# Optimization experiments

Measured on AMD Instinct MI355X. Metric: run time of the kernel, lower is better.

Reference implementation:

```python
import jax, jax.numpy as jnp
import numpy as np

N, E, G = 10000, 160000, 64
F, C1, C2, C3, K, NC = 128, 128, 256, 512, 5, 10


def setup_inputs() -> dict:
    key = jax.random.key(0)
    ks = jax.random.split(key, 12)
    s = 0.05
    return {
        "x": jax.random.normal(ks[0], (N, F), dtype=jnp.float32),
        "edge_index": jax.random.randint(ks[1], (2, E), 0, N, dtype=jnp.int64),
        "batch": jnp.sort(jax.random.randint(ks[2], (N,), 0, G, dtype=jnp.int64)),
        "W_cheb": jax.random.normal(ks[3], (K, F, C1), dtype=jnp.float32) * s,
        "b_cheb": jnp.zeros((C1,), jnp.float32),
        "W_g1": jax.random.normal(ks[4], (C1, C2), dtype=jnp.float32) * s,
        "b_g1": jnp.zeros((C2,), jnp.float32),
        "W_g2": jax.random.normal(ks[5], (C2, C3), dtype=jnp.float32) * s,
        "b_g2": jnp.zeros((C3,), jnp.float32),
        "w_gate": jax.random.normal(ks[6], (C3, 1), dtype=jnp.float32) * s,
        "b_gate": jnp.zeros((1,), jnp.float32),
        "W_fc": jax.random.normal(ks[7], (C3, NC), dtype=jnp.float32) * s,
        "b_fc": jnp.zeros((NC,), jnp.float32),
    }


def _deg_inv_sqrt(deg):
    return jnp.where(deg > 0, jax.lax.rsqrt(jnp.maximum(deg, 1e-12)), 0.0)


def cheb_conv(x, src, dst, W, b):
    # PyG ChebConv, sym normalization, lambda_max=2 => scaled Laplacian = -D^-1/2 A D^-1/2
    ones = jnp.ones((src.shape[0],), x.dtype)
    deg = jax.ops.segment_sum(ones, src, num_segments=N)
    dinv = _deg_inv_sqrt(deg)
    w = -(dinv[src] * dinv[dst])  # [E]

    def prop(h):
        return jax.ops.segment_sum(w[:, None] * h[src], dst, num_segments=N)

    tx0 = x
    tx1 = prop(x)
    out = tx0 @ W[0] + tx1 @ W[1]
    for k in range(2, W.shape[0]):
        tx2 = 2.0 * prop(tx1) - tx0
        out = out + tx2 @ W[k]
        tx0, tx1 = tx1, tx2
    return out + b


def gcn_conv(x, src, dst, W, b):
    # PyG GCNConv: add self-loops, sym norm D~^-1/2 (A+I) D~^-1/2, transform then aggregate
    loop = jnp.arange(N, dtype=src.dtype)
    src_a = jnp.concatenate([src, loop])
    dst_a = jnp.concatenate([dst, loop])
    ones = jnp.ones((src_a.shape[0],), x.dtype)
    deg = jax.ops.segment_sum(ones, dst_a, num_segments=N)
    dinv = _deg_inv_sqrt(deg)
    norm = dinv[src_a] * dinv[dst_a]  # [E+N]
    h = x @ W
    return jax.ops.segment_sum(norm[:, None] * h[src_a], dst_a, num_segments=N) + b


def attention_pool(x, batch, w_gate, b_gate):
    logits = (x @ w_gate + b_gate)[:, 0]  # [N]
    m = jax.ops.segment_max(logits, batch, num_segments=G)
    e = jnp.exp(logits - m[batch])
    s = jax.ops.segment_sum(e, batch, num_segments=G)
    alpha = e / s[batch]
    return jax.ops.segment_sum(alpha[:, None] * x, batch, num_segments=G)  # [G, C3]


def reference(x, edge_index, batch, W_cheb, b_cheb, W_g1, b_g1, W_g2, b_g2,
              w_gate, b_gate, W_fc, b_fc):
    src, dst = edge_index[0], edge_index[1]
    h = jax.nn.relu(cheb_conv(x, src, dst, W_cheb, b_cheb))
    h = jax.nn.relu(gcn_conv(h, src, dst, W_g1, b_g1))
    h = jax.nn.relu(gcn_conv(h, src, dst, W_g2, b_g2))
    g = attention_pool(h, batch, w_gate, b_gate)
    logits = g @ W_fc + b_fc
    return jax.nn.log_softmax(logits, axis=1)
```

## Files before the change

### kernel.cpp

```cpp
#include <hip/hip_runtime.h>
#include <hip/hip_bf16.h>
#include <math.h>

#define N_NODES 10000
#define N_EDGES 160000
#define N_GRAPHS 64
#define F_IN    128
#define C1_DIM  128
#define C2_DIM  256
#define C3_DIM  512
#define K_CHEB  5
#define NCLS    10
#define TC      (K_CHEB * F_IN)

typedef short v8s __attribute__((ext_vector_type(8)));
typedef float v4f __attribute__((ext_vector_type(4)));

static __device__ __forceinline__ unsigned short f2bf(float f) {
    unsigned u = __float_as_uint(f);
    unsigned r = (u + 0x7FFFu + ((u >> 16) & 1u)) >> 16;
    return (unsigned short)r;
}
static __device__ __forceinline__ float bf_lo(unsigned u) { return __uint_as_float(u << 16); }
static __device__ __forceinline__ float bf_hi(unsigned u) { return __uint_as_float(u & 0xFFFF0000u); }

__global__ void count_kernel(const int* __restrict__ src, const int* __restrict__ dst,
                             int* __restrict__ cnt_s, int* __restrict__ cnt_d, int E) {
    int e = blockIdx.x * blockDim.x + threadIdx.x;
    if (e >= E) return;
    atomicAdd(&cnt_s[src[e]], 1);
    atomicAdd(&cnt_d[dst[e]], 1);
}

__global__ __launch_bounds__(256) void scan_dinv_kernel(
        const int* __restrict__ cnt_s, const int* __restrict__ cnt_d,
        int* __restrict__ rowptr, float* __restrict__ dinv_c, float* __restrict__ dinv_g, int n) {
    __shared__ int sums[256];
    int tid = threadIdx.x;
    int chunk = (n + 255) / 256;
    int s0 = tid * chunk, s1 = min(n, s0 + chunk);
    int loc = 0;
    for (int i = s0; i < s1; i++) {
        int cd = cnt_d[i];
        loc += cd;
        int cs = cnt_s[i];
        dinv_c[i] = (cs > 0) ? rsqrtf((float)cs) : 0.0f;
        dinv_g[i] = rsqrtf((float)cd + 1.0f);
    }
    sums[tid] = loc;
    __syncthreads();
    for (int off = 1; off < 256; off <<= 1) {
        int t = (tid >= off) ? sums[tid - off] : 0;
        __syncthreads();
        sums[tid] += t;
        __syncthreads();
    }
    int pre = sums[tid] - loc;
    for (int i = s0; i < s1; i++) { rowptr[i] = pre; pre += cnt_d[i]; }
    if (tid == 255) rowptr[n] = pre;
}

__global__ void fill_kernel(const int* __restrict__ src, const int* __restrict__ dst,
                            const float* __restrict__ dinv_c, const float* __restrict__ dinv_g,
                            const int* __restrict__ rowptr, int* __restrict__ fillc,
                            int* __restrict__ col, float* __restrict__ wch,
                            float* __restrict__ nrm, int E) {
    int e = blockIdx.x * blockDim.x + threadIdx.x;
    if (e >= E) return;
    int s = src[e], d = dst[e];
    int pos = rowptr[d] + atomicAdd(&fillc[d], 1);
    col[pos] = s;
    wch[pos] = -(dinv_c[s] * dinv_c[d]);
    nrm[pos] = dinv_g[s] * dinv_g[d];
}

#define PREP_A (N_NODES * 64)
#define PREP_B (TC * C1_DIM)
#define PREP_C (C1_DIM * C2_DIM)
#define PREP_D (C2_DIM * C3_DIM)
#define PREP_TOTAL (PREP_A + PREP_B + PREP_C + PREP_D + N_NODES)
__global__ void prep_kernel(const float* __restrict__ x, unsigned short* __restrict__ tcat,
                            const float* __restrict__ Wcheb, unsigned short* __restrict__ Wcb_t,
                            const float* __restrict__ Wg1, unsigned short* __restrict__ Wg1_t,
                            const float* __restrict__ Wg2, unsigned short* __restrict__ Wg2_t,
                            const int* __restrict__ batch, int* __restrict__ gptr) {
    int id = blockIdx.x * blockDim.x + threadIdx.x;
    if (id < PREP_A) {
        int n = id >> 6, f = (id & 63) * 2;
        float2 v = *(const float2*)(x + (size_t)n * F_IN + f);
        ushort2 o; o.x = f2bf(v.x); o.y = f2bf(v.y);
        *(ushort2*)(tcat + (size_t)n * TC + f) = o;
        return;
    }
    id -= PREP_A;
    if (id < PREP_B) {
        int n = id % C1_DIM, k = id / C1_DIM;
        Wcb_t[(size_t)n * TC + k] = f2bf(Wcheb[(size_t)k * C1_DIM + n]);
        return;
    }
    id -= PREP_B;
    if (id < PREP_C) {
        int n = id % C2_DIM, k = id / C2_DIM;
        Wg1_t[(size_t)n * C1_DIM + k] = f2bf(Wg1[(size_t)k * C2_DIM + n]);
        return;
    }
    id -= PREP_C;
    if (id < PREP_D) {
        int n = id % C3_DIM, k = id / C3_DIM;
        Wg2_t[(size_t)n * C2_DIM + k] = f2bf(Wg2[(size_t)k * C3_DIM + n]);
        return;
    }
    id -= PREP_D;
    int i = id;
    int b = batch[i];
    if (i == 0) { for (int g = 0; g <= b; g++) gptr[g] = 0; }
    else {
        int bp = batch[i - 1];
        for (int g = bp + 1; g <= b; g++) gptr[g] = i;
    }
    if (i == N_NODES - 1) { for (int g = b + 1; g <= N_GRAPHS; g++) gptr[g] = N_NODES; }
}

__global__ __launch_bounds__(256) void gather_cheb_bf(
        const unsigned short* __restrict__ tb,
        const int* __restrict__ rowptr, const int* __restrict__ col,
        const float* __restrict__ ew,
        const unsigned short* __restrict__ base,
        float alpha, float beta,
        unsigned short* __restrict__ outc,
        int n) {
    int w = (blockIdx.x * blockDim.x + threadIdx.x) >> 6;
    int lane = threadIdx.x & 63;
    if (w >= n) return;
    float a0 = 0.0f, a1 = 0.0f;
    int rs = rowptr[w], re = rowptr[w + 1];
    for (int b = rs; b < re; b += 64) {
        int cl = 0; float wl = 0.0f;
        if (b + lane < re) { cl = col[b + lane]; wl = ew[b + lane]; }
        int nk4 = (min(64, re - b) + 3) & ~3;
        for (int j = 0; j < nk4; j += 4) {
            int s0 = __shfl(cl, j), s1 = __shfl(cl, j + 1);
            int s2 = __shfl(cl, j + 2), s3 = __shfl(cl, j + 3);
            float w0 = __shfl(wl, j), w1 = __shfl(wl, j + 1);
            float w2 = __shfl(wl, j + 2), w3 = __shfl(wl, j + 3);
            unsigned u0 = ((const unsigned*)(tb + (size_t)s0 * TC))[lane];
            unsigned u1 = ((const unsigned*)(tb + (size_t)s1 * TC))[lane];
            unsigned u2 = ((const unsigned*)(tb + (size_t)s2 * TC))[lane];
            unsigned u3 = ((const unsigned*)(tb + (size_t)s3 * TC))[lane];
            a0 += w0 * bf_lo(u0) + w1 * bf_lo(u1) + w2 * bf_lo(u2) + w3 * bf_lo(u3);
            a1 += w0 * bf_hi(u0) + w1 * bf_hi(u1) + w2 * bf_hi(u2) + w3 * bf_hi(u3);
        }
    }
    if (base) {
        unsigned ub = ((const unsigned*)(base + (size_t)w * TC))[lane];
        a0 = alpha * a0 + beta * bf_lo(ub);
        a1 = alpha * a1 + beta * bf_hi(ub);
    } else {
        a0 *= alpha; a1 *= alpha;
    }
    ushort2 o; o.x = f2bf(a0); o.y = f2bf(a1);
    *(ushort2*)(outc + (size_t)w * TC + lane * 2) = o;
}

template<int FPL>
__global__ __launch_bounds__(256) void gather_gcn_pre(
        const unsigned short* __restrict__ tb, const int* __restrict__ rowptr,
        const int* __restrict__ col, const float* __restrict__ ew,
        const float* __restrict__ dinv, unsigned short* __restrict__ z, int n) {
    const int C = FPL * 64;
    int w = (blockIdx.x * blockDim.x + threadIdx.x) >> 6;
    int lane = threadIdx.x & 63;
    if (w >= n) return;
    float acc[FPL];
    #pragma unroll
    for (int q = 0; q < FPL; q++) acc[q] = 0.0f;
    int rs = rowptr[w], re = rowptr[w + 1];
    for (int b = rs; b < re; b += 64) {
        int cl = 0; float wl = 0.0f;
        if (b + lane < re) { cl = col[b + lane]; wl = ew[b + lane]; }
        int nk4 = (min(64, re - b) + 3) & ~3;
        for (int j = 0; j < nk4; j += 4) {
            int s0 = __shfl(cl, j), s1 = __shfl(cl, j + 1);
            int s2 = __shfl(cl, j + 2), s3 = __shfl(cl, j + 3);
            float w0 = __shfl(wl, j), w1 = __shfl(wl, j + 1);
            float w2 = __shfl(wl, j + 2), w3 = __shfl(wl, j + 3);
            if constexpr (FPL == 2) {
                unsigned u0 = ((const unsigned*)(tb + (size_t)s0 * C))[lane];
                unsigned u1 = ((const unsigned*)(tb + (size_t)s1 * C))[lane];
                unsigned u2 = ((const unsigned*)(tb + (size_t)s2 * C))[lane];
                unsigned u3 = ((const unsigned*)(tb + (size_t)s3 * C))[lane];
                acc[0] += w0 * bf_lo(u0) + w1 * bf_lo(u1) + w2 * bf_lo(u2) + w3 * bf_lo(u3);
                acc[1] += w0 * bf_hi(u0) + w1 * bf_hi(u1) + w2 * bf_hi(u2) + w3 * bf_hi(u3);
            } else {
                uint2 u0 = ((const uint2*)(tb + (size_t)s0 * C))[lane];
                uint2 u1 = ((const uint2*)(tb + (size_t)s1 * C))[lane];
                uint2 u2 = ((const uint2*)(tb + (size_t)s2 * C))[lane];
                uint2 u3 = ((const uint2*)(tb + (size_t)s3 * C))[lane];
                acc[0] += w0 * bf_lo(u0.x) + w1 * bf_lo(u1.x) + w2 * bf_lo(u2.x) + w3 * bf_lo(u3.x);
                acc[1] += w0 * bf_hi(u0.x) + w1 * bf_hi(u1.x) + w2 * bf_hi(u2.x) + w3 * bf_hi(u3.x);
                acc[2] += w0 * bf_lo(u0.y) + w1 * bf_lo(u1.y) + w2 * bf_lo(u2.y) + w3 * bf_lo(u3.y);
                acc[3] += w0 * bf_hi(u0.y) + w1 * bf_hi(u1.y) + w2 * bf_hi(u2.y) + w3 * bf_hi(u3.y);
            }
        }
    }
    float sn = dinv[w] * dinv[w];
    if constexpr (FPL == 2) {
        unsigned u = ((const unsigned*)(tb + (size_t)w * C))[lane];
        acc[0] += sn * bf_lo(u); acc[1] += sn * bf_hi(u);
        ushort2 o; o.x = f2bf(acc[0]); o.y = f2bf(acc[1]);
        *(ushort2*)(z + (size_t)w * C + lane * 2) = o;
    } else {
        uint2 u = ((const uint2*)(tb + (size_t)w * C))[lane];
        acc[0] += sn * bf_lo(u.x); acc[1] += sn * bf_hi(u.x);
        acc[2] += sn * bf_lo(u.y); acc[3] += sn * bf_hi(u.y);
        ushort4 o; o.x = f2bf(acc[0]); o.y = f2bf(acc[1]);
        o.z = f2bf(acc[2]); o.w = f2bf(acc[3]);
        *(ushort4*)(z + (size_t)w * C + lane * 4) = o;
    }
}

__global__ __launch_bounds__(256) void gemm_bf16(
        const unsigned short* __restrict__ A, const unsigned short* __restrict__ Bt,
        const float* __restrict__ bias, float* __restrict__ Cf,
        unsigned short* __restrict__ Cb, int M, int K, int N, int relu) {
    int m0 = blockIdx.y * 64, n0 = blockIdx.x * 128;
    int wave = threadIdx.x >> 6, lane = threadIdx.x & 63;
    int wm = (wave & 1) * 32, wn = (wave >> 1) * 64;
    int l15 = lane & 15, quad = lane >> 4;

    v4f acc[2][4];
    #pragma unroll
    for (int i = 0; i < 2; i++)
        #pragma unroll
        for (int j = 0; j < 4; j++) acc[i][j] = (v4f){0.f, 0.f, 0.f, 0.f};

    const unsigned short* Ab[2]; bool av[2];
    #pragma unroll
    for (int i = 0; i < 2; i++) {
        int row = m0 + wm + i * 16 + l15;
        av[i] = row < M;
        Ab[i] = A + (size_t)(av[i] ? row : 0) * K + quad * 8;
    }
    const unsigned short* Bb[4];
    #pragma unroll
    for (int j = 0; j < 4; j++) {
        int coln = n0 + wn + j * 16 + l15;
        Bb[j] = Bt + (size_t)coln * K + quad * 8;
    }
    const v8s zero8 = {0, 0, 0, 0, 0, 0, 0, 0};

    for (int k0 = 0; k0 < K; k0 += 32) {
        v8s a[2], b[4];
        #pragma unroll
        for (int i = 0; i < 2; i++) a[i] = av[i] ? *(const v8s*)(Ab[i] + k0) : zero8;
        #pragma unroll
        for (int j = 0; j < 4; j++) b[j] = *(const v8s*)(Bb[j] + k0);
        #pragma unroll
        for (int i = 0; i < 2; i++)
            #pragma unroll
            for (int j = 0; j < 4; j++)
                acc[i][j] = __builtin_amdgcn_mfma_f32_16x16x32_bf16(a[i], b[j], acc[i][j], 0, 0, 0);
    }

    #pragma unroll
    for (int j = 0; j < 4; j++) {
        int coln = n0 + wn + j * 16 + l15;
        float bv = bias ? bias[coln] : 0.0f;
        #pragma unroll
        for (int i = 0; i < 2; i++) {
            int rbase = m0 + wm + i * 16 + quad * 4;
            #pragma unroll
            for (int r = 0; r < 4; r++) {
                int row = rbase + r;
                if (row >= M) continue;
                float v = acc[i][j][r] + bv;
                if (relu) v = fmaxf(v, 0.0f);
                if (Cf) Cf[(size_t)row * N + coln] = v;
                else    Cb[(size_t)row * N + coln] = f2bf(v);
            }
        }
    }
}

__global__ void gate_kernel(const float* __restrict__ h3, const float* __restrict__ wg,
                            const float* __restrict__ bg, float* __restrict__ logits, int n) {
    int node = blockIdx.x * 4 + (threadIdx.x >> 6);
    int lane = threadIdx.x & 63;
    if (node >= n) return;
    float s = 0.0f;
    #pragma unroll
    for (int i = 0; i < 8; i++) {
        int c = i * 64 + lane;
        s += h3[(size_t)node * C3_DIM + c] * wg[c];
    }
    #pragma unroll
    for (int off = 32; off > 0; off >>= 1) s += __shfl_down(s, off);
    if (lane == 0) logits[node] = s + bg[0];
}

__global__ __launch_bounds__(256) void pool_stats(float* __restrict__ logits,
                                                  const int* __restrict__ gptr,
                                                  float* __restrict__ pooled) {
    __shared__ float red[256];
    int g = blockIdx.x, tid = threadIdx.x;
    int gs = gptr[g], ge = gptr[g + 1];
    pooled[(size_t)g * C3_DIM + tid] = 0.0f;
    pooled[(size_t)g * C3_DIM + 256 + tid] = 0.0f;
    float m = -INFINITY;
    for (int i = gs + tid; i < ge; i += 256) m = fmaxf(m, logits[i]);
    red[tid] = m; __syncthreads();
    for (int off = 128; off > 0; off >>= 1) {
        if (tid < off) red[tid] = fmaxf(red[tid], red[tid + off]);
        __syncthreads();
    }
    m = red[0]; __syncthreads();
    float s = 0.0f;
    for (int i = gs + tid; i < ge; i += 256) s += expf(logits[i] - m);
    red[tid] = s; __syncthreads();
    for (int off = 128; off > 0; off >>= 1) {
        if (tid < off) red[tid] += red[tid + off];
        __syncthreads();
    }
    s = red[0];
    float sinv = (s > 0.0f) ? 1.0f / s : 0.0f;
    for (int i = gs + tid; i < ge; i += 256)
        logits[i] = expf(logits[i] - m) * sinv;
}

__global__ __launch_bounds__(256) void pool_partial(const float* __restrict__ h3,
        const float* __restrict__ alpha, const int* __restrict__ gptr,
        float* __restrict__ pooled) {
    int g = blockIdx.x, ch = blockIdx.y, sl = blockIdx.z;
    int gs = gptr[g], ge = gptr[g + 1];
    int cnt = ge - gs;
    int i0 = gs + (cnt * sl) / 8;
    int i1 = gs + (cnt * (sl + 1)) / 8;
    int c = ch * 256 + threadIdx.x;
    float acc = 0.0f;
    for (int i = i0; i < i1; i++)
        acc += alpha[i] * h3[(size_t)i * C3_DIM + c];
    if (i1 > i0) atomicAdd(&pooled[(size_t)g * C3_DIM + c], acc);
}

__global__ void fc_kernel(const float* __restrict__ pooled, const float* __restrict__ Wfc,
                          const float* __restrict__ bfc, float* __restrict__ out) {
    int g = blockIdx.x;
    int t = threadIdx.x;
    float acc = -INFINITY;
    if (t < NCLS) {
        acc = bfc[t];
        for (int k = 0; k < C3_DIM; k++)
            acc += pooled[(size_t)g * C3_DIM + k] * Wfc[k * NCLS + t];
    }
    float m = acc;
    #pragma unroll
    for (int off = 8; off > 0; off >>= 1) m = fmaxf(m, __shfl_xor(m, off, 16));
    float e = (t < NCLS) ? expf(acc - m) : 0.0f;
    float s = e;
    #pragma unroll
    for (int off = 8; off > 0; off >>= 1) s += __shfl_xor(s, off, 16);
    if (t < NCLS) out[g * NCLS + t] = acc - m - logf(s);
}

extern "C" void kernel_launch(void* const* d_in, const int* in_sizes, int n_in,
                              void* d_out, int out_size, void* d_ws, size_t ws_size,
                              hipStream_t stream) {
    const float* x      = (const float*)d_in[0];
    const int*   ei     = (const int*)d_in[1];
    const int*   batch  = (const int*)d_in[2];
    const float* W_cheb = (const float*)d_in[3];
    const float* b_cheb = (const float*)d_in[4];
    const float* W_g1   = (const float*)d_in[5];
    const float* b_g1   = (const float*)d_in[6];
    const float* W_g2   = (const float*)d_in[7];
    const float* b_g2   = (const float*)d_in[8];
    const float* w_gate = (const float*)d_in[9];
    const float* b_gate = (const float*)d_in[10];
    const float* W_fc   = (const float*)d_in[11];
    const float* b_fc   = (const float*)d_in[12];
    const int* src = ei;
    const int* dst = ei + N_EDGES;
    float* out = (float*)d_out;

    const int N = N_NODES, E = N_EDGES, G = N_GRAPHS;

    char* Wp = (char*)d_ws;
    auto alloc = [&](size_t bytes) {
        void* p = Wp;
        Wp += (bytes + 255) & ~(size_t)255;
        return p;
    };
    int*   cnt3    = (int*)alloc((size_t)3 * N * 4);
    int*   cnt_s   = cnt3;
    int*   cnt_d   = cnt3 + N;
    int*   fillc   = cnt3 + 2 * N;
    int*   rowptr  = (int*)alloc((N + 1) * 4);
    int*   col     = (int*)alloc(E * 4);
    float* wch     = (float*)alloc(E * 4);
    float* nrm     = (float*)alloc(E * 4);
    float* dinv_c  = (float*)alloc(N * 4);
    float* dinv_g  = (float*)alloc(N * 4);
    unsigned short* tcat  = (unsigned short*)alloc((size_t)N * TC * 2);
    unsigned short* h1b   = (unsigned short*)alloc((size_t)N * C1_DIM * 2);
    unsigned short* z1b   = (unsigned short*)alloc((size_t)N * C1_DIM * 2);
    unsigned short* h2b   = (unsigned short*)alloc((size_t)N * C2_DIM * 2);
    unsigned short* z2b   = (unsigned short*)alloc((size_t)N * C2_DIM * 2);
    float* h3      = (float*)alloc((size_t)N * C3_DIM * 4);
    unsigned short* Wcb_t = (unsigned short*)alloc((size_t)TC * C1_DIM * 2);
    unsigned short* Wg1_t = (unsigned short*)alloc((size_t)C1_DIM * C2_DIM * 2);
    unsigned short* Wg2_t = (unsigned short*)alloc((size_t)C2_DIM * C3_DIM * 2);
    float* logits  = (float*)alloc(N * 4);
    int*   gptr    = (int*)alloc((G + 1) * 4);
    float* pooled  = (float*)alloc((size_t)G * C3_DIM * 4);

    dim3 blk(256);
    auto cdiv = [](int a, int b) { return (a + b - 1) / b; };

    hipLaunchKernelGGL(prep_kernel, dim3(cdiv(PREP_TOTAL, 256)), blk, 0, stream,
                       x, tcat, W_cheb, Wcb_t, W_g1, Wg1_t, W_g2, Wg2_t, batch, gptr);

    hipMemsetAsync(cnt3, 0, (size_t)3 * N * sizeof(int), stream);
    hipLaunchKernelGGL(count_kernel, dim3(cdiv(E, 256)), blk, 0, stream, src, dst, cnt_s, cnt_d, E);
    hipLaunchKernelGGL(scan_dinv_kernel, dim3(1), blk, 0, stream, cnt_s, cnt_d, rowptr, dinv_c, dinv_g, N);
    hipLaunchKernelGGL(fill_kernel, dim3(cdiv(E, 256)), blk, 0, stream,
                       src, dst, dinv_c, dinv_g, rowptr, fillc, col, wch, nrm, E);

    const int NWB = cdiv(N, 4);

    hipLaunchKernelGGL(gather_cheb_bf, dim3(NWB), blk, 0, stream,
                       tcat + 0 * F_IN, rowptr, col, wch,
                       (const unsigned short*)nullptr, 1.0f, 0.0f, tcat + 1 * F_IN, N);
    hipLaunchKernelGGL(gather_cheb_bf, dim3(NWB), blk, 0, stream,
                       tcat + 1 * F_IN, rowptr, col, wch,
                       tcat + 0 * F_IN, 2.0f, -1.0f, tcat + 2 * F_IN, N);
    hipLaunchKernelGGL(gather_cheb_bf, dim3(NWB), blk, 0, stream,
                       tcat + 2 * F_IN, rowptr, col, wch,
                       tcat + 1 * F_IN, 2.0f, -1.0f, tcat + 3 * F_IN, N);
    hipLaunchKernelGGL(gather_cheb_bf, dim3(NWB), blk, 0, stream,
                       tcat + 3 * F_IN, rowptr, col, wch,
                       tcat + 2 * F_IN, 2.0f, -1.0f, tcat + 4 * F_IN, N);

    hipLaunchKernelGGL(gemm_bf16, dim3(C1_DIM / 128, cdiv(N, 64)), blk, 0, stream,
                       tcat, Wcb_t, b_cheb, (float*)nullptr, h1b, N, TC, C1_DIM, 1);

    hipLaunchKernelGGL(gather_gcn_pre<2>, dim3(NWB), blk, 0, stream,
                       h1b, rowptr, col, nrm, dinv_g, z1b, N);
    hipLaunchKernelGGL(gemm_bf16, dim3(C2_DIM / 128, cdiv(N, 64)), blk, 0, stream,
                       z1b, Wg1_t, b_g1, (float*)nullptr, h2b, N, C1_DIM, C2_DIM, 1);

    hipLaunchKernelGGL(gather_gcn_pre<4>, dim3(NWB), blk, 0, stream,
                       h2b, rowptr, col, nrm, dinv_g, z2b, N);
    hipLaunchKernelGGL(gemm_bf16, dim3(C3_DIM / 128, cdiv(N, 64)), blk, 0, stream,
                       z2b, Wg2_t, b_g2, h3, (unsigned short*)nullptr, N, C2_DIM, C3_DIM, 1);

    hipLaunchKernelGGL(gate_kernel, dim3(cdiv(N, 4)), blk, 0, stream, h3, w_gate, b_gate, logits, N);
    hipLaunchKernelGGL(pool_stats, dim3(G), blk, 0, stream, logits, gptr, pooled);
    hipLaunchKernelGGL(pool_partial, dim3(G, C3_DIM / 256, 8), blk, 0, stream,
                       h3, logits, gptr, pooled);

    hipLaunchKernelGGL(fc_kernel, dim3(G), dim3(64), 0, stream, pooled, W_fc, b_fc, out);
}
```

Before: 312.6 us.

## Fuse gate into GEMM epilogue, store h3 in bf16, merge degree counting into prep

Several changes at once. The edge degree counting and logits zeroing move into the prep kernel, and the scan now runs from LDS. The dinv arrays are dropped and degrees are computed on the fly in fill and gather. The gather loops are unrolled to 8 loads in flight. The GEMM is templated on column tiles, using a narrower tile for the first layer, and the final GEMM writes h3 as bf16 while computing the gate logits in its epilogue with atomics, which removes the separate gate kernel and halves h3 traffic in pooling. Risks: the gate bias is dropped (harmless here since softmax cancels it), atomic logit accumulation order varies, and bf16 h3 lowers pooling precision.

```diff
diff --git a/kernel.cpp b/kernel.cpp
--- a/kernel.cpp
+++ b/kernel.cpp
@@ -24,29 +24,81 @@
 static __device__ __forceinline__ float bf_lo(unsigned u) { return __uint_as_float(u << 16); }
 static __device__ __forceinline__ float bf_hi(unsigned u) { return __uint_as_float(u & 0xFFFF0000u); }
 
-__global__ void count_kernel(const int* __restrict__ src, const int* __restrict__ dst,
-                             int* __restrict__ cnt_s, int* __restrict__ cnt_d, int E) {
-    int e = blockIdx.x * blockDim.x + threadIdx.x;
-    if (e >= E) return;
-    atomicAdd(&cnt_s[src[e]], 1);
-    atomicAdd(&cnt_d[dst[e]], 1);
-}
-
-__global__ __launch_bounds__(256) void scan_dinv_kernel(
-        const int* __restrict__ cnt_s, const int* __restrict__ cnt_d,
-        int* __restrict__ rowptr, float* __restrict__ dinv_c, float* __restrict__ dinv_g, int n) {
+#define PREP_A (N_NODES * 64)
+#define PREP_B (TC * C1_DIM)
+#define PREP_C (C1_DIM * C2_DIM)
+#define PREP_D (C2_DIM * C3_DIM)
+#define PREP_E N_NODES
+#define PREP_F N_NODES
+#define PREP_G N_EDGES
+#define PREP_TOTAL (PREP_A + PREP_B + PREP_C + PREP_D + PREP_E + PREP_F + PREP_G)
+__global__ void prep_kernel(const float* __restrict__ x, unsigned short* __restrict__ tcat,
+                            const float* __restrict__ Wcheb, unsigned short* __restrict__ Wcb_t,
+                            const float* __restrict__ Wg1, unsigned short* __restrict__ Wg1_t,
+                            const float* __restrict__ Wg2, unsigned short* __restrict__ Wg2_t,
+                            const int* __restrict__ batch, int* __restrict__ gptr,
+                            float* __restrict__ logits,
+                            const int* __restrict__ src, const int* __restrict__ dst,
+                            int* __restrict__ cnt_s, int* __restrict__ cnt_d) {
+    int id = blockIdx.x * blockDim.x + threadIdx.x;
+    if (id < PREP_A) {
+        int n = id >> 6, f = (id & 63) * 2;
+        float2 v = *(const float2*)(x + (size_t)n * F_IN + f);
+        ushort2 o; o.x = f2bf(v.x); o.y = f2bf(v.y);
+        *(ushort2*)(tcat + (size_t)n * TC + f) = o;
+        return;
+    }
+    id -= PREP_A;
+    if (id < PREP_B) {
+        int n = id % C1_DIM, k = id / C1_DIM;
+        Wcb_t[(size_t)n * TC + k] = f2bf(Wcheb[(size_t)k * C1_DIM + n]);
+        return;
+    }
+    id -= PREP_B;
+    if (id < PREP_C) {
+        int n = id % C2_DIM, k = id / C2_DIM;
+        Wg1_t[(size_t)n * C1_DIM + k] = f2bf(Wg1[(size_t)k * C2_DIM + n]);
+        return;
+    }
+    id -= PREP_C;
+    if (id < PREP_D) {
+        int n = id % C3_DIM, k = id / C3_DIM;
+        Wg2_t[(size_t)n * C2_DIM + k] = f2bf(Wg2[(size_t)k * C3_DIM + n]);
+        return;
+    }
+    id -= PREP_D;
+    if (id < PREP_E) {
+        int i = id;
+        int b = batch[i];
+        if (i == 0) { for (int g = 0; g <= b; g++) gptr[g] = 0; }
+        else {
+            int bp = batch[i - 1];
+            for (int g = bp + 1; g <= b; g++) gptr[g] = i;
+        }
+        if (i == N_NODES - 1) { for (int g = b + 1; g <= N_GRAPHS; g++) gptr[g] = N_NODES; }
+        return;
+    }
+    id -= PREP_E;
+    if (id < PREP_F) { logits[id] = 0.0f; return; }
+    id -= PREP_F;
+    if (id < PREP_G) {
+        atomicAdd(&cnt_s[src[id]], 1);
+        atomicAdd(&cnt_d[dst[id]], 1);
+    }
+}
+
+__global__ __launch_bounds__(256) void scan_kernel(const int* __restrict__ cnt_d,
+                                                   int* __restrict__ rowptr, int n) {
+    __shared__ int ldsc[N_NODES];
     __shared__ int sums[256];
     int tid = threadIdx.x;
+    for (int i = tid; i < n; i += 256) ldsc[i] = cnt_d[i];
+    __syncthreads();
     int chunk = (n + 255) / 256;
     int s0 = tid * chunk, s1 = min(n, s0 + chunk);
+    if (s0 > n) s0 = n;
     int loc = 0;
-    for (int i = s0; i < s1; i++) {
-        int cd = cnt_d[i];
-        loc += cd;
-        int cs = cnt_s[i];
-        dinv_c[i] = (cs > 0) ? rsqrtf((float)cs) : 0.0f;
-        dinv_g[i] = rsqrtf((float)cd + 1.0f);
-    }
+    for (int i = s0; i < s1; i++) loc += ldsc[i];
     sums[tid] = loc;
     __syncthreads();
     for (int off = 1; off < 256; off <<= 1) {
@@ -56,12 +108,14 @@
         __syncthreads();
     }
     int pre = sums[tid] - loc;
-    for (int i = s0; i < s1; i++) { rowptr[i] = pre; pre += cnt_d[i]; }
+    for (int i = s0; i < s1; i++) { int v = ldsc[i]; ldsc[i] = pre; pre += v; }
+    __syncthreads();
+    for (int i = tid; i < n; i += 256) rowptr[i] = ldsc[i];
     if (tid == 255) rowptr[n] = pre;
 }
 
 __global__ void fill_kernel(const int* __restrict__ src, const int* __restrict__ dst,
-                            const float* __restrict__ dinv_c, const float* __restrict__ dinv_g,
+                            const int* __restrict__ cnt_s, const int* __restrict__ cnt_d,
                             const int* __restrict__ rowptr, int* __restrict__ fillc,
                             int* __restrict__ col, float* __restrict__ wch,
                             float* __restrict__ nrm, int E) {
@@ -70,65 +124,18 @@
     int s = src[e], d = dst[e];
     int pos = rowptr[d] + atomicAdd(&fillc[d], 1);
     col[pos] = s;
-    wch[pos] = -(dinv_c[s] * dinv_c[d]);
-    nrm[pos] = dinv_g[s] * dinv_g[d];
-}
-
-#define PREP_A (N_NODES * 64)
-#define PREP_B (TC * C1_DIM)
-#define PREP_C (C1_DIM * C2_DIM)
-#define PREP_D (C2_DIM * C3_DIM)
-#define PREP_TOTAL (PREP_A + PREP_B + PREP_C + PREP_D + N_NODES)
-__global__ void prep_kernel(const float* __restrict__ x, unsigned short* __restrict__ tcat,
-                            const float* __restrict__ Wcheb, unsigned short* __restrict__ Wcb_t,
-                            const float* __restrict__ Wg1, unsigned short* __restrict__ Wg1_t,
-                            const float* __restrict__ Wg2, unsigned short* __restrict__ Wg2_t,
-                            const int* __restrict__ batch, int* __restrict__ gptr) {
-    int id = blockIdx.x * blockDim.x + threadIdx.x;
-    if (id < PREP_A) {
-        int n = id >> 6, f = (id & 63) * 2;
-        float2 v = *(const float2*)(x + (size_t)n * F_IN + f);
-        ushort2 o; o.x = f2bf(v.x); o.y = f2bf(v.y);
-        *(ushort2*)(tcat + (size_t)n * TC + f) = o;
-        return;
-    }
-    id -= PREP_A;
-    if (id < PREP_B) {
-        int n = id % C1_DIM, k = id / C1_DIM;
-        Wcb_t[(size_t)n * TC + k] = f2bf(Wcheb[(size_t)k * C1_DIM + n]);
-        return;
-    }
-    id -= PREP_B;
-    if (id < PREP_C) {
-        int n = id % C2_DIM, k = id / C2_DIM;
-        Wg1_t[(size_t)n * C1_DIM + k] = f2bf(Wg1[(size_t)k * C2_DIM + n]);
-        return;
-    }
-    id -= PREP_C;
-    if (id < PREP_D) {
-        int n = id % C3_DIM, k = id / C3_DIM;
-        Wg2_t[(size_t)n * C2_DIM + k] = f2bf(Wg2[(size_t)k * C3_DIM + n]);
-        return;
-    }
-    id -= PREP_D;
-    int i = id;
-    int b = batch[i];
-    if (i == 0) { for (int g = 0; g <= b; g++) gptr[g] = 0; }
-    else {
-        int bp = batch[i - 1];
-        for (int g = bp + 1; g <= b; g++) gptr[g] = i;
-    }
-    if (i == N_NODES - 1) { for (int g = b + 1; g <= N_GRAPHS; g++) gptr[g] = N_NODES; }
+    int cs = cnt_s[s], cd = cnt_s[d];
+    float ds = (cs > 0) ? rsqrtf((float)cs) : 0.0f;
+    float dd = (cd > 0) ? rsqrtf((float)cd) : 0.0f;
+    wch[pos] = -(ds * dd);
+    nrm[pos] = rsqrtf((float)cnt_d[s] + 1.0f) * rsqrtf((float)cnt_d[d] + 1.0f);
 }
 
 __global__ __launch_bounds__(256) void gather_cheb_bf(
-        const unsigned short* __restrict__ tb,
-        const int* __restrict__ rowptr, const int* __restrict__ col,
-        const float* __restrict__ ew,
-        const unsigned short* __restrict__ base,
-        float alpha, float beta,
-        unsigned short* __restrict__ outc,
-        int n) {
+        const unsigned short* __restrict__ tb, const int* __restrict__ rowptr,
+        const int* __restrict__ col, const float* __restrict__ ew,
+        const unsigned short* __restrict__ base, float alpha, float beta,
+        unsigned short* __restrict__ outc, int n) {
     int w = (blockIdx.x * blockDim.x + threadIdx.x) >> 6;
     int lane = threadIdx.x & 63;
     if (w >= n) return;
@@ -137,18 +144,15 @@
     for (int b = rs; b < re; b += 64) {
         int cl = 0; float wl = 0.0f;
         if (b + lane < re) { cl = col[b + lane]; wl = ew[b + lane]; }
-        int nk4 = (min(64, re - b) + 3) & ~3;
-        for (int j = 0; j < nk4; j += 4) {
-            int s0 = __shfl(cl, j), s1 = __shfl(cl, j + 1);
-            int s2 = __shfl(cl, j + 2), s3 = __shfl(cl, j + 3);
-            float w0 = __shfl(wl, j), w1 = __shfl(wl, j + 1);
-            float w2 = __shfl(wl, j + 2), w3 = __shfl(wl, j + 3);
-            unsigned u0 = ((const unsigned*)(tb + (size_t)s0 * TC))[lane];
-            unsigned u1 = ((const unsigned*)(tb + (size_t)s1 * TC))[lane];
-            unsigned u2 = ((const unsigned*)(tb + (size_t)s2 * TC))[lane];
-            unsigned u3 = ((const unsigned*)(tb + (size_t)s3 * TC))[lane];
-            a0 += w0 * bf_lo(u0) + w1 * bf_lo(u1) + w2 * bf_lo(u2) + w3 * bf_lo(u3);
-            a1 += w0 * bf_hi(u0) + w1 * bf_hi(u1) + w2 * bf_hi(u2) + w3 * bf_hi(u3);
+        int nk8 = (min(64, re - b) + 7) & ~7;
+        for (int j = 0; j < nk8; j += 8) {
+            int ss[8]; float ww[8]; unsigned uu[8];
+            #pragma unroll
+            for (int q = 0; q < 8; q++) { ss[q] = __shfl(cl, j + q); ww[q] = __shfl(wl, j + q); }
+            #pragma unroll
+            for (int q = 0; q < 8; q++) uu[q] = ((const unsigned*)(tb + (size_t)ss[q] * TC))[lane];
+            #pragma unroll
+            for (int q = 0; q < 8; q++) { a0 += ww[q] * bf_lo(uu[q]); a1 += ww[q] * bf_hi(uu[q]); }
         }
     }
     if (base) {
@@ -166,7 +170,7 @@
 __global__ __launch_bounds__(256) void gather_gcn_pre(
         const unsigned short* __restrict__ tb, const int* __restrict__ rowptr,
         const int* __restrict__ col, const float* __restrict__ ew,
-        const float* __restrict__ dinv, unsigned short* __restrict__ z, int n) {
+        const int* __restrict__ cnt_d, unsigned short* __restrict__ z, int n) {
     const int C = FPL * 64;
     int w = (blockIdx.x * blockDim.x + threadIdx.x) >> 6;
     int lane = threadIdx.x & 63;
@@ -178,32 +182,33 @@
     for (int b = rs; b < re; b += 64) {
         int cl = 0; float wl = 0.0f;
         if (b + lane < re) { cl = col[b + lane]; wl = ew[b + lane]; }
-        int nk4 = (min(64, re - b) + 3) & ~3;
-        for (int j = 0; j < nk4; j += 4) {
-            int s0 = __shfl(cl, j), s1 = __shfl(cl, j + 1);
-            int s2 = __shfl(cl, j + 2), s3 = __shfl(cl, j + 3);
-            float w0 = __shfl(wl, j), w1 = __shfl(wl, j + 1);
-            float w2 = __shfl(wl, j + 2), w3 = __shfl(wl, j + 3);
+        int nk8 = (min(64, re - b) + 7) & ~7;
+        for (int j = 0; j < nk8; j += 8) {
+            int ss[8]; float ww[8];
+            #pragma unroll
+            for (int q = 0; q < 8; q++) { ss[q] = __shfl(cl, j + q); ww[q] = __shfl(wl, j + q); }
             if constexpr (FPL == 2) {
-                unsigned u0 = ((const unsigned*)(tb + (size_t)s0 * C))[lane];
-                unsigned u1 = ((const unsigned*)(tb + (size_t)s1 * C))[lane];
-                unsigned u2 = ((const unsigned*)(tb + (size_t)s2 * C))[lane];
-                unsigned u3 = ((const unsigned*)(tb + (size_t)s3 * C))[lane];
-                acc[0] += w0 * bf_lo(u0) + w1 * bf_lo(u1) + w2 * bf_lo(u2) + w3 * bf_lo(u3);
-                acc[1] += w0 * bf_hi(u0) + w1 * bf_hi(u1) + w2 * bf_hi(u2) + w3 * bf_hi(u3);
+                unsigned uu[8];
+                #pragma unroll
+                for (int q = 0; q < 8; q++) uu[q] = ((const unsigned*)(tb + (size_t)ss[q] * C))[lane];
+                #pragma unroll
+                for (int q = 0; q < 8; q++) {
+                    acc[0] += ww[q] * bf_lo(uu[q]);
+                    acc[1] += ww[q] * bf_hi(uu[q]);
+                }
             } else {
-                uint2 u0 = ((const uint2*)(tb + (size_t)s0 * C))[lane];
-                uint2 u1 = ((const uint2*)(tb + (size_t)s1 * C))[lane];
-                uint2 u2 = ((const uint2*)(tb + (size_t)s2 * C))[lane];
-                uint2 u3 = ((const uint2*)(tb + (size_t)s3 * C))[lane];
-                acc[0] += w0 * bf_lo(u0.x) + w1 * bf_lo(u1.x) + w2 * bf_lo(u2.x) + w3 * bf_lo(u3.x);
-                acc[1] += w0 * bf_hi(u0.x) + w1 * bf_hi(u1.x) + w2 * bf_hi(u2.x) + w3 * bf_hi(u3.x);
-                acc[2] += w0 * bf_lo(u0.y) + w1 * bf_lo(u1.y) + w2 * bf_lo(u2.y) + w3 * bf_lo(u3.y);
-                acc[3] += w0 * bf_hi(u0.y) + w1 * bf_hi(u1.y) + w2 * bf_hi(u2.y) + w3 * bf_hi(u3.y);
+                uint2 uu[8];
+                #pragma unroll
+                for (int q = 0; q < 8; q++) uu[q] = ((const uint2*)(tb + (size_t)ss[q] * C))[lane];
+                #pragma unroll
+                for (int q = 0; q < 8; q++) {
+                    acc[0] += ww[q] * bf_lo(uu[q].x); acc[1] += ww[q] * bf_hi(uu[q].x);
+                    acc[2] += ww[q] * bf_lo(uu[q].y); acc[3] += ww[q] * bf_hi(uu[q].y);
+                }
             }
         }
     }
-    float sn = dinv[w] * dinv[w];
+    float sn = 1.0f / (float)(cnt_d[w] + 1);
     if constexpr (FPL == 2) {
         unsigned u = ((const unsigned*)(tb + (size_t)w * C))[lane];
         acc[0] += sn * bf_lo(u); acc[1] += sn * bf_hi(u);
@@ -219,20 +224,22 @@
     }
 }
 
+template<int JT>
 __global__ __launch_bounds__(256) void gemm_bf16(
         const unsigned short* __restrict__ A, const unsigned short* __restrict__ Bt,
         const float* __restrict__ bias, float* __restrict__ Cf,
-        unsigned short* __restrict__ Cb, int M, int K, int N, int relu) {
-    int m0 = blockIdx.y * 64, n0 = blockIdx.x * 128;
+        unsigned short* __restrict__ Cb, const float* __restrict__ wg,
+        float* __restrict__ logits, int M, int K, int N, int relu) {
+    int m0 = blockIdx.y * 64, n0 = blockIdx.x * (JT * 32);
     int wave = threadIdx.x >> 6, lane = threadIdx.x & 63;
-    int wm = (wave & 1) * 32, wn = (wave >> 1) * 64;
+    int wm = (wave & 1) * 32, wn = (wave >> 1) * (JT * 16);
     int l15 = lane & 15, quad = lane >> 4;
 
-    v4f acc[2][4];
+    v4f acc[2][JT];
     #pragma unroll
     for (int i = 0; i < 2; i++)
         #pragma unroll
-        for (int j = 0; j < 4; j++) acc[i][j] = (v4f){0.f, 0.f, 0.f, 0.f};
+        for (int j = 0; j < JT; j++) acc[i][j] = (v4f){0.f, 0.f, 0.f, 0.f};
 
     const unsigned short* Ab[2]; bool av[2];
     #pragma unroll
@@ -241,61 +248,57 @@
         av[i] = row < M;
         Ab[i] = A + (size_t)(av[i] ? row : 0) * K + quad * 8;
     }
-    const unsigned short* Bb[4];
-    #pragma unroll
-    for (int j = 0; j < 4; j++) {
+    const unsigned short* Bb[JT];
+    #pragma unroll
+    for (int j = 0; j < JT; j++) {
         int coln = n0 + wn + j * 16 + l15;
         Bb[j] = Bt + (size_t)coln * K + quad * 8;
     }
     const v8s zero8 = {0, 0, 0, 0, 0, 0, 0, 0};
 
     for (int k0 = 0; k0 < K; k0 += 32) {
-        v8s a[2], b[4];
+        v8s a[2], b[JT];
         #pragma unroll
         for (int i = 0; i < 2; i++) a[i] = av[i] ? *(const v8s*)(Ab[i] + k0) : zero8;
         #pragma unroll
-        for (int j = 0; j < 4; j++) b[j] = *(const v8s*)(Bb[j] + k0);
+        for (int j = 0; j < JT; j++) b[j] = *(const v8s*)(Bb[j] + k0);
         #pragma unroll
         for (int i = 0; i < 2; i++)
             #pragma unroll
-            for (int j = 0; j < 4; j++)
+            for (int j = 0; j < JT; j++)
                 acc[i][j] = __builtin_amdgcn_mfma_f32_16x16x32_bf16(a[i], b[j], acc[i][j], 0, 0, 0);
     }
 
-    #pragma unroll
-    for (int j = 0; j < 4; j++) {
+    float bv[JT], wgj[JT];
+    #pragma unroll
+    for (int j = 0; j < JT; j++) {
         int coln = n0 + wn + j * 16 + l15;
-        float bv = bias ? bias[coln] : 0.0f;
+        bv[j] = bias[coln];
+        wgj[j] = wg ? wg[coln] : 0.0f;
+    }
+    #pragma unroll
+    for (int i = 0; i < 2; i++) {
         #pragma unroll
-        for (int i = 0; i < 2; i++) {
-            int rbase = m0 + wm + i * 16 + quad * 4;
-            #pragma unroll
-            for (int r = 0; r < 4; r++) {
-                int row = rbase + r;
-                if (row >= M) continue;
-                float v = acc[i][j][r] + bv;
+        for (int r = 0; r < 4; r++) {
+            int row = m0 + wm + i * 16 + quad * 4 + r;
+            if (row >= M) continue;
+            float gval = 0.0f;
+            #pragma unroll
+            for (int j = 0; j < JT; j++) {
+                int coln = n0 + wn + j * 16 + l15;
+                float v = acc[i][j][r] + bv[j];
                 if (relu) v = fmaxf(v, 0.0f);
                 if (Cf) Cf[(size_t)row * N + coln] = v;
                 else    Cb[(size_t)row * N + coln] = f2bf(v);
+                gval += v * wgj[j];
+            }
+            if (wg) {
+                #pragma unroll
+                for (int off = 1; off < 16; off <<= 1) gval += __shfl_xor(gval, off);
+                if (l15 == 0) atomicAdd(&logits[row], gval);
             }
         }
     }
-}
-
-__global__ void gate_kernel(const float* __restrict__ h3, const float* __restrict__ wg,
-                            const float* __restrict__ bg, float* __restrict__ logits, int n) {
-    int node = blockIdx.x * 4 + (threadIdx.x >> 6);
-    int lane = threadIdx.x & 63;
-    if (node >= n) return;
-    float s = 0.0f;
-    #pragma unroll
-    for (int i = 0; i < 8; i++) {
-        int c = i * 64 + lane;
-        s += h3[(size_t)node * C3_DIM + c] * wg[c];
-    }
-    #pragma unroll
-    for (int off = 32; off > 0; off >>= 1) s += __shfl_down(s, off);
-    if (lane == 0) logits[node] = s + bg[0];
 }
 
 __global__ __launch_bounds__(256) void pool_stats(float* __restrict__ logits,
@@ -327,19 +330,25 @@
         logits[i] = expf(logits[i] - m) * sinv;
 }
 
-__global__ __launch_bounds__(256) void pool_partial(const float* __restrict__ h3,
+__global__ __launch_bounds__(256) void pool_partial(const unsigned short* __restrict__ h3b,
         const float* __restrict__ alpha, const int* __restrict__ gptr,
         float* __restrict__ pooled) {
-    int g = blockIdx.x, ch = blockIdx.y, sl = blockIdx.z;
+    int g = blockIdx.x, sl = blockIdx.y, tid = threadIdx.x;
     int gs = gptr[g], ge = gptr[g + 1];
     int cnt = ge - gs;
     int i0 = gs + (cnt * sl) / 8;
     int i1 = gs + (cnt * (sl + 1)) / 8;
-    int c = ch * 256 + threadIdx.x;
-    float acc = 0.0f;
-    for (int i = i0; i < i1; i++)
-        acc += alpha[i] * h3[(size_t)i * C3_DIM + c];
-    if (i1 > i0) atomicAdd(&pooled[(size_t)g * C3_DIM + c], acc);
+    float a0 = 0.0f, a1 = 0.0f;
+    for (int i = i0; i < i1; i++) {
+        float al = alpha[i];
+        unsigned u = ((const unsigned*)(h3b + (size_t)i * C3_DIM))[tid];
+        a0 += al * bf_lo(u);
+        a1 += al * bf_hi(u);
+    }
+    if (i1 > i0) {
+        atomicAdd(&pooled[(size_t)g * C3_DIM + tid * 2 + 0], a0);
+        atomicAdd(&pooled[(size_t)g * C3_DIM + tid * 2 + 1], a1);
+    }
 }
 
 __global__ void fc_kernel(const float* __restrict__ pooled, const float* __restrict__ Wfc,
@@ -375,7 +384,6 @@
     const float* W_g2   = (const float*)d_in[7];
     const float* b_g2   = (const float*)d_in[8];
     const float* w_gate = (const float*)d_in[9];
-    const float* b_gate = (const float*)d_in[10];
     const float* W_fc   = (const float*)d_in[11];
     const float* b_fc   = (const float*)d_in[12];
     const int* src = ei;
@@ -398,14 +406,12 @@
     int*   col     = (int*)alloc(E * 4);
     float* wch     = (float*)alloc(E * 4);
     float* nrm     = (float*)alloc(E * 4);
-    float* dinv_c  = (float*)alloc(N * 4);
-    float* dinv_g  = (float*)alloc(N * 4);
     unsigned short* tcat  = (unsigned short*)alloc((size_t)N * TC * 2);
     unsigned short* h1b   = (unsigned short*)alloc((size_t)N * C1_DIM * 2);
     unsigned short* z1b   = (unsigned short*)alloc((size_t)N * C1_DIM * 2);
     unsigned short* h2b   = (unsigned short*)alloc((size_t)N * C2_DIM * 2);
     unsigned short* z2b   = (unsigned short*)alloc((size_t)N * C2_DIM * 2);
-    float* h3      = (float*)alloc((size_t)N * C3_DIM * 4);
+    unsigned short* h3b   = (unsigned short*)alloc((size_t)N * C3_DIM * 2);
     unsigned short* Wcb_t = (unsigned short*)alloc((size_t)TC * C1_DIM * 2);
     unsigned short* Wg1_t = (unsigned short*)alloc((size_t)C1_DIM * C2_DIM * 2);
     unsigned short* Wg2_t = (unsigned short*)alloc((size_t)C2_DIM * C3_DIM * 2);
@@ -416,14 +422,14 @@
     dim3 blk(256);
     auto cdiv = [](int a, int b) { return (a + b - 1) / b; };
 
+    hipMemsetAsync(cnt3, 0, (size_t)3 * N * sizeof(int), stream);
     hipLaunchKernelGGL(prep_kernel, dim3(cdiv(PREP_TOTAL, 256)), blk, 0, stream,
-                       x, tcat, W_cheb, Wcb_t, W_g1, Wg1_t, W_g2, Wg2_t, batch, gptr);
-
-    hipMemsetAsync(cnt3, 0, (size_t)3 * N * sizeof(int), stream);
-    hipLaunchKernelGGL(count_kernel, dim3(cdiv(E, 256)), blk, 0, stream, src, dst, cnt_s, cnt_d, E);
-    hipLaunchKernelGGL(scan_dinv_kernel, dim3(1), blk, 0, stream, cnt_s, cnt_d, rowptr, dinv_c, dinv_g, N);
+                       x, tcat, W_cheb, Wcb_t, W_g1, Wg1_t, W_g2, Wg2_t,
+                       batch, gptr, logits, src, dst, cnt_s, cnt_d);
+
+    hipLaunchKernelGGL(scan_kernel, dim3(1), blk, 0, stream, cnt_d, rowptr, N);
     hipLaunchKernelGGL(fill_kernel, dim3(cdiv(E, 256)), blk, 0, stream,
-                       src, dst, dinv_c, dinv_g, rowptr, fillc, col, wch, nrm, E);
+                       src, dst, cnt_s, cnt_d, rowptr, fillc, col, wch, nrm, E);
 
     const int NWB = cdiv(N, 4);
 
@@ -440,23 +446,24 @@
                        tcat + 3 * F_IN, rowptr, col, wch,
                        tcat + 2 * F_IN, 2.0f, -1.0f, tcat + 4 * F_IN, N);
 
-    hipLaunchKernelGGL(gemm_bf16, dim3(C1_DIM / 128, cdiv(N, 64)), blk, 0, stream,
-                       tcat, Wcb_t, b_cheb, (float*)nullptr, h1b, N, TC, C1_DIM, 1);
+    hipLaunchKernelGGL(gemm_bf16<2>, dim3(C1_DIM / 64, cdiv(N, 64)), blk, 0, stream,
+                       tcat, Wcb_t, b_cheb, (float*)nullptr, h1b,
+                       (const float*)nullptr, (float*)nullptr, N, TC, C1_DIM, 1);
 
     hipLaunchKernelGGL(gather_gcn_pre<2>, dim3(NWB), blk, 0, stream,
-                       h1b, rowptr, col, nrm, dinv_g, z1b, N);
-    hipLaunchKernelGGL(gemm_bf16, dim3(C2_DIM / 128, cdiv(N, 64)), blk, 0, stream,
-                       z1b, Wg1_t, b_g1, (float*)nullptr, h2b, N, C1_DIM, C2_DIM, 1);
+                       h1b, rowptr, col, nrm, cnt_d, z1b, N);
+    hipLaunchKernelGGL(gemm_bf16<4>, dim3(C2_DIM / 128, cdiv(N, 64)), blk, 0, stream,
+                       z1b, Wg1_t, b_g1, (float*)nullptr, h2b,
+                       (const float*)nullptr, (float*)nullptr, N, C1_DIM, C2_DIM, 1);
 
     hipLaunchKernelGGL(gather_gcn_pre<4>, dim3(NWB), blk, 0, stream,
-                       h2b, rowptr, col, nrm, dinv_g, z2b, N);
-    hipLaunchKernelGGL(gemm_bf16, dim3(C3_DIM / 128, cdiv(N, 64)), blk, 0, stream,
-                       z2b, Wg2_t, b_g2, h3, (unsigned short*)nullptr, N, C2_DIM, C3_DIM, 1);
-
-    hipLaunchKernelGGL(gate_kernel, dim3(cdiv(N, 4)), blk, 0, stream, h3, w_gate, b_gate, logits, N);
+                       h2b, rowptr, col, nrm, cnt_d, z2b, N);
+    hipLaunchKernelGGL(gemm_bf16<4>, dim3(C3_DIM / 128, cdiv(N, 64)), blk, 0, stream,
+                       z2b, Wg2_t, b_g2, (float*)nullptr, h3b,
+                       w_gate, logits, N, C2_DIM, C3_DIM, 1);
+
     hipLaunchKernelGGL(pool_stats, dim3(G), blk, 0, stream, logits, gptr, pooled);
-    hipLaunchKernelGGL(pool_partial, dim3(G, C3_DIM / 256, 8), blk, 0, stream,
-                       h3, logits, gptr, pooled);
+    hipLaunchKernelGGL(pool_partial, dim3(G, 8), blk, 0, stream, h3b, logits, gptr, pooled);
 
     hipLaunchKernelGGL(fc_kernel, dim3(G), dim3(64), 0, stream, pooled, W_fc, b_fc, out);
 }
```

After: 265.4 us. 15.1% less time.
